# Optimization experiments

Measured on AMD Instinct MI355X. Metric: run time of the kernel, lower is better.

The kernel has to match this reference:

```python
import jax, jax.numpy as jnp
import numpy as np

B, T, D, H, L = 256, 1024, 64, 128, 2

def _lstm_layer(x, h0, c0, w_ih, w_hh, b):
    # x: [B,T,Din]; w_ih: [4H,Din]; w_hh: [4H,H]; b: [4H]
    xg = jnp.einsum('btd,gd->btg', x, w_ih) + b  # precompute input-to-gate GEMM: [B,T,4H]
    def step(carry, xt):
        h, c = carry
        g = xt + h @ w_hh.T                       # [B,4H], torch gate order i,f,g,o
        i, f, gg, o = jnp.split(g, 4, axis=-1)
        c = jax.nn.sigmoid(f) * c + jax.nn.sigmoid(i) * jnp.tanh(gg)
        h = jax.nn.sigmoid(o) * jnp.tanh(c)
        return (h, c), h
    _, hs = jax.lax.scan(step, (h0, c0), jnp.swapaxes(xg, 0, 1))  # hs: [T,B,H]
    return jnp.swapaxes(hs, 0, 1)


def setup_inputs() -> dict:
    key = jax.random.key(0)
    ks = jax.random.split(key, 12)
    s = 1.0 / np.sqrt(H)
    u = lambda k, shp: jax.random.uniform(k, shp, jnp.float32, -s, s)
    return {
        'x': jax.random.normal(ks[0], (B, T, D), jnp.float32),
        'h0': jax.random.normal(ks[1], (L, B, H), jnp.float32),
        'w_ih_0': u(ks[2], (4 * H, D)),
        'w_hh_0': u(ks[3], (4 * H, H)),
        'b_0': u(ks[4], (4 * H,)),
        'w_ih_1': u(ks[5], (4 * H, H)),
        'w_hh_1': u(ks[6], (4 * H, H)),
        'b_1': u(ks[7], (4 * H,)),
        'fc_w': u(ks[8], (1, H)),
        'fc_b': u(ks[9], (1,)),
    }


def reference(x, h0, w_ih_0, w_hh_0, b_0, w_ih_1, w_hh_1, b_1, fc_w, fc_b):
    c0 = jnp.zeros((x.shape[0], w_hh_0.shape[1]), x.dtype)  # c0 = zeros as in original
    h = _lstm_layer(x, h0[0], c0, w_ih_0, w_hh_0, b_0)
    h = _lstm_layer(h, h0[1], c0, w_ih_1, w_hh_1, b_1)
    return h[:, -1, :] @ fc_w.T + fc_b  # fc2 on last timestep -> [B,1]
```

## Files before the change

### kernel.cpp

```cpp
#include <hip/hip_runtime.h>
#include <math.h>

#define NB  256
#define T   1024
#define DIN 64
#define H   128
#define G4  512
#define NBT (NB * T)
#define TG4 (T * G4)

typedef __attribute__((ext_vector_type(4))) float    f32x4;
typedef __attribute__((ext_vector_type(8))) _Float16 f16x8;
typedef __attribute__((ext_vector_type(4))) _Float16 f16x4;
typedef __attribute__((ext_vector_type(2))) _Float16 f16x2;

#define DPPQ(v, CTRL) __int_as_float(__builtin_amdgcn_update_dpp(0, __float_as_int(v), (CTRL), 0xf, 0xf, true))
#define MFMA16(A, B, C) __builtin_amdgcn_mfma_f32_16x16x32_f16((A), (B), (C), 0, 0, 0)

__device__ __forceinline__ float tanhf_(float x) { return 2.0f / (1.0f + __expf(-2.0f * x)) - 1.0f; }

__device__ __forceinline__ void wg_barrier() {
    asm volatile("s_waitcnt lgkmcnt(0)" ::: "memory");
    __builtin_amdgcn_s_barrier();
}

__device__ __forceinline__ f16x8 cvt8(const float* p) {
    float4 v0 = *(const float4*)p;
    float4 v1 = *(const float4*)(p + 4);
    return (f16x8){(_Float16)v0.x, (_Float16)v0.y, (_Float16)v0.z, (_Float16)v0.w,
                   (_Float16)v1.x, (_Float16)v1.y, (_Float16)v1.z, (_Float16)v1.w};
}

template<int K, int AH>
__global__ __launch_bounds__(256, 2)
void gemm_pp(const void* __restrict__ A, const float* __restrict__ W,
             _Float16* __restrict__ O)
{
    __shared__ _Float16 __align__(16) sA[128][136];
    __shared__ _Float16 __align__(16) sW[128][72];

    const int m0 = blockIdx.x << 7;
    const int j = threadIdx.x;
    const int lane = j & 63, wv = j >> 6;
    const int wm = wv >> 1, wn = wv & 1;
    const int q = lane >> 4, n16 = lane & 15;
    const int bb = m0 >> 10, s0 = m0 & (T - 1);
    const size_t bO = (size_t)bb * TG4;

    if constexpr (AH) {
        const _Float16* Ah = (const _Float16*)A;
        #pragma unroll
        for (int it = 0; it < 8; ++it) {
            int idx = j + it * 256;
            int kp = idx & 63, sblk = idx >> 6;
            f16x8 xv8 = *(const f16x8*)(Ah + bO + (size_t)kp * 2048
                                        + (size_t)(s0 + sblk * 4) * 2);
            #pragma unroll
            for (int d = 0; d < 4; ++d)
                *(f16x2*)&sA[sblk * 4 + d][2 * kp] = (f16x2){xv8[2 * d], xv8[2 * d + 1]};
        }
    } else {
        const float* Af = (const float*)A;
        #pragma unroll
        for (int it = 0; it < 8; ++it) {
            int idx = j + it * 256;
            int r = idx >> 4, kc = (idx & 15) << 2;
            float4 va = *(const float4*)(Af + (size_t)(m0 + r) * K + kc);
            *(f16x4*)&sA[r][kc] = (f16x4){(_Float16)va.x, (_Float16)va.y,
                                          (_Float16)va.z, (_Float16)va.w};
        }
    }

    for (int nb = 0; nb < 4; ++nb) {
        f32x4 acc[4][4];
        #pragma unroll
        for (int a = 0; a < 4; ++a)
            #pragma unroll
            for (int bq = 0; bq < 4; ++bq) acc[a][bq] = (f32x4){0.f, 0.f, 0.f, 0.f};

        #pragma unroll
        for (int kp = 0; kp < K / 64; ++kp) {
            __syncthreads();
            #pragma unroll
            for (int it = 0; it < 8; ++it) {
                int idx = j + it * 256;
                int r = idx >> 4, kc = (idx & 15) << 2;
                int n = (nb << 7) + r, pn = (n & 3) * 128 + (n >> 2);
                float4 vw = *(const float4*)(W + (size_t)pn * K + kp * 64 + kc);
                *(f16x4*)&sW[r][kc] = (f16x4){(_Float16)vw.x, (_Float16)vw.y,
                                              (_Float16)vw.z, (_Float16)vw.w};
            }
            __syncthreads();
            #pragma unroll
            for (int kh = 0; kh < 2; ++kh) {
                const int kk = kh * 32 + q * 8;
                f16x8 a[4], bf[4];
                #pragma unroll
                for (int mt = 0; mt < 4; ++mt)
                    a[mt] = *(const f16x8*)&sA[wm * 64 + mt * 16 + n16][kp * 64 + kk];
                #pragma unroll
                for (int nt = 0; nt < 4; ++nt)
                    bf[nt] = *(const f16x8*)&sW[wn * 64 + nt * 16 + n16][kk];
                #pragma unroll
                for (int nt = 0; nt < 4; ++nt)
                    #pragma unroll
                    for (int mt = 0; mt < 4; ++mt)
                        acc[mt][nt] = MFMA16(a[mt], bf[nt], acc[mt][nt]);
            }
        }
        const int N0 = (nb << 7) + wn * 64;
        const int nA = N0 + n16, nBc = N0 + 32 + n16;
        const int grpA = (nA >> 7) * 64 + ((nA >> 5) & 3) * 16 + (nA & 15);
        const int grpB = (nBc >> 7) * 64 + ((nBc >> 5) & 3) * 16 + (nBc & 15);
        #pragma unroll
        for (int mt = 0; mt < 4; ++mt) {
            int srow = (m0 + wm * 64 + mt * 16 + q * 4) & (T - 1);
            f16x8 pkA = {(_Float16)acc[mt][0][0], (_Float16)acc[mt][1][0],
                         (_Float16)acc[mt][0][1], (_Float16)acc[mt][1][1],
                         (_Float16)acc[mt][0][2], (_Float16)acc[mt][1][2],
                         (_Float16)acc[mt][0][3], (_Float16)acc[mt][1][3]};
            f16x8 pkB = {(_Float16)acc[mt][2][0], (_Float16)acc[mt][3][0],
                         (_Float16)acc[mt][2][1], (_Float16)acc[mt][3][1],
                         (_Float16)acc[mt][2][2], (_Float16)acc[mt][3][2],
                         (_Float16)acc[mt][2][3], (_Float16)acc[mt][3][3]};
            *(f16x8*)(O + bO + (size_t)grpA * 2048 + (size_t)srow * 2) = pkA;
            *(f16x8*)(O + bO + (size_t)grpB * 2048 + (size_t)srow * 2) = pkB;
        }
    }
}

__global__ __launch_bounds__(256, 1)
void lstm_scan(const _Float16* __restrict__ xg, const float* __restrict__ whh,
               const float* __restrict__ bias, const float* __restrict__ h0g,
               _Float16* hist, const float* __restrict__ fcw,
               const float* __restrict__ fcb, float* __restrict__ out, int dofc)
{
    __shared__ _Float16 __align__(16) hb[2][128];
    __shared__ float lds_r[128];

    const int b = blockIdx.x;
    const int t = threadIdx.x;
    const int lane = t & 63, v = t >> 6;
    const int l15 = lane & 15, q = lane >> 4;
    const int u = l15 >> 2, gg = l15 & 3;

    f16x8 wf[8][4];
    #pragma unroll
    for (int jj = 0; jj < 8; ++jj) {
        const int n  = 128 * v + 16 * jj + l15;
        const int pn = (n & 3) * 128 + (n >> 2);
        const float* wr = whh + (size_t)pn * H;
        #pragma unroll
        for (int kt = 0; kt < 4; ++kt)
            wf[jj][kt] = cvt8(wr + 32 * kt + q * 8);
    }
    const int huA = 32 * v + 8 * q + u;
    const int huB = huA + 4;
    const float bjA = bias[gg * 128 + huA];
    const float bjB = bias[gg * 128 + huB];

    const bool  isg = (gg == 2);
    const float nsc = isg ? -2.0f : -1.0f;
    const float va  = isg ?  2.0f :  1.0f;
    const float vb  = isg ? -1.0f :  0.0f;
    const bool  sq0 = (q & 1) != 0;
    const bool  sq1 = (q & 2) != 0;
    const bool  wlane = gg < 2;
    const int   hu_own = wlane ? (gg ? huB : huA) : huA;

    if (t < H) hb[0][t] = (_Float16)h0g[(size_t)b * H + t];

    float cA = 0.f, cB = 0.f, hOwn = 0.f;

    const _Float16* xgp = xg + (size_t)b * TG4 + (size_t)(v * 64 + q * 16 + l15) * 2048;
    f16x8 xr0 = *(const f16x8*)(xgp + 0);
    f16x8 xr1 = *(const f16x8*)(xgp + 8);

    _Float16* hp = hist ? hist + (size_t)b * TG4 + (size_t)(hu_own >> 1) * 2048 + (hu_own & 1)
                        : (_Float16*)0;

    __syncthreads();

    const f32x4 z = (f32x4){0.f, 0.f, 0.f, 0.f};

    for (int sb = 0; sb < T; sb += 8) {
        #pragma unroll
        for (int ss = 0; ss < 8; ++ss) {
            const int s = sb + ss;
            const int p = s & 1;

            f16x8 xcur = (ss < 4) ? xr0 : xr1;
            float xA = (float)xcur[(ss & 3) * 2];
            float xB = (float)xcur[(ss & 3) * 2 + 1];

            f16x8 af[4];
            #pragma unroll
            for (int kt = 0; kt < 4; ++kt)
                af[kt] = *(const f16x8*)(&hb[p][32 * kt + q * 8]);

            f32x4 a[8];
            #pragma unroll
            for (int jj = 0; jj < 8; ++jj)
                a[jj] = MFMA16(af[0], wf[jj][0], z);
            #pragma unroll
            for (int kt = 1; kt < 4; ++kt)
                #pragma unroll
                for (int jj = 0; jj < 8; ++jj)
                    a[jj] = MFMA16(af[kt], wf[jj][kt], a[jj]);

            float gA = (sq0 ? (sq1 ? a[6][0] : a[2][0]) : (sq1 ? a[4][0] : a[0][0]))
                       + xA + bjA;
            float gB = (sq0 ? (sq1 ? a[7][0] : a[3][0]) : (sq1 ? a[5][0] : a[1][0]))
                       + xB + bjB;

            if (ss == 3) { int i0 = sb + 8;  if (i0 > T - 4) i0 = T - 4; xr0 = *(const f16x8*)(xgp + (size_t)i0 * 2); }
            if (ss == 7) { int i1 = sb + 12; if (i1 > T - 4) i1 = T - 4; xr1 = *(const f16x8*)(xgp + (size_t)i1 * 2); }

            float uA  = 1.0f / (1.0f + __expf(nsc * gA));
            float vlA = fmaf(uA, va, vb);
            float uB  = 1.0f / (1.0f + __expf(nsc * gB));
            float vlB = fmaf(uB, va, vb);

            float niA = DPPQ(vlA, 0x00), nfA = DPPQ(vlA, 0x55);
            float ngA = DPPQ(vlA, 0xAA), noA = DPPQ(vlA, 0xFF);
            float niB = DPPQ(vlB, 0x00), nfB = DPPQ(vlB, 0x55);
            float ngB = DPPQ(vlB, 0xAA), noB = DPPQ(vlB, 0xFF);

            cA = nfA * cA + niA * ngA;
            cB = nfB * cB + niB * ngB;

            if (wlane) {
                float cs = gg ? cB : cA;
                float ns = gg ? noB : noA;
                float h  = ns * tanhf_(cs);
                hOwn = h;
                hb[p ^ 1][hu_own] = (_Float16)h;
                if (hp) hp[(size_t)s * 2] = (_Float16)h;
            }

            wg_barrier();
        }
    }

    if (dofc) {
        if (wlane) lds_r[hu_own] = hOwn * fcw[hu_own];
        __syncthreads();
        if (t == 0) {
            float s_ = fcb[0];
            for (int k = 0; k < H; ++k) s_ += lds_r[k];
            out[b] = s_;
        }
    }
}

extern "C" void kernel_launch(void* const* d_in, const int* in_sizes, int n_in,
                              void* d_out, int out_size, void* d_ws, size_t ws_size,
                              hipStream_t stream)
{
    const float* x    = (const float*)d_in[0];
    const float* h0   = (const float*)d_in[1];
    const float* wih0 = (const float*)d_in[2];
    const float* whh0 = (const float*)d_in[3];
    const float* b0   = (const float*)d_in[4];
    const float* wih1 = (const float*)d_in[5];
    const float* whh1 = (const float*)d_in[6];
    const float* b1   = (const float*)d_in[7];
    const float* fcw  = (const float*)d_in[8];
    const float* fcb  = (const float*)d_in[9];
    float* out = (float*)d_out;

    _Float16* xg = (_Float16*)d_ws;

    gemm_pp<64, 0><<<NBT / 128, 256, 0, stream>>>(x, wih0, xg);
    lstm_scan<<<NB, 256, 0, stream>>>(xg, whh0, b0, h0, xg,
                                      nullptr, nullptr, nullptr, 0);
    gemm_pp<128, 1><<<NBT / 128, 256, 0, stream>>>(xg, wih1, xg);
    lstm_scan<<<NB, 256, 0, stream>>>(xg, whh1, b1, h0 + (size_t)NB * H,
                                      nullptr, fcw, fcb, out, 1);
}
```

Before: 1.280 ms.

## Split LSTM scan across 512 threads and fold bias into input GEMM

The recurrent scan kernel now runs 512 threads per batch row (8 waves), so each wave holds half as many W_hh fragments and issues 16 MFMAs per step instead of 32. Each lane now handles a single gate element instead of two. The gate bias is added in the input-projection GEMM epilogue instead of per step in the scan. This shortens the serial per-step critical path, at the cost of a wider workgroup barrier across 8 waves each step and bias being rounded into fp16 with the projection.

```diff
diff --git a/kernel.cpp b/kernel.cpp
--- a/kernel.cpp
+++ b/kernel.cpp
@@ -16,6 +16,7 @@
 
 #define DPPQ(v, CTRL) __int_as_float(__builtin_amdgcn_update_dpp(0, __float_as_int(v), (CTRL), 0xf, 0xf, true))
 #define MFMA16(A, B, C) __builtin_amdgcn_mfma_f32_16x16x32_f16((A), (B), (C), 0, 0, 0)
+#define PN(n) ((((n) & 3) * 128) + ((n) >> 2))
 
 __device__ __forceinline__ float tanhf_(float x) { return 2.0f / (1.0f + __expf(-2.0f * x)) - 1.0f; }
 
@@ -34,7 +35,7 @@
 template<int K, int AH>
 __global__ __launch_bounds__(256, 2)
 void gemm_pp(const void* __restrict__ A, const float* __restrict__ W,
-             _Float16* __restrict__ O)
+             const float* __restrict__ bias, _Float16* __restrict__ O)
 {
     __shared__ _Float16 __align__(16) sA[128][136];
     __shared__ _Float16 __align__(16) sW[128][72];
@@ -85,7 +86,7 @@
             for (int it = 0; it < 8; ++it) {
                 int idx = j + it * 256;
                 int r = idx >> 4, kc = (idx & 15) << 2;
-                int n = (nb << 7) + r, pn = (n & 3) * 128 + (n >> 2);
+                int n = (nb << 7) + r, pn = PN(n);
                 float4 vw = *(const float4*)(W + (size_t)pn * K + kp * 64 + kc);
                 *(f16x4*)&sW[r][kc] = (f16x4){(_Float16)vw.x, (_Float16)vw.y,
                                               (_Float16)vw.z, (_Float16)vw.w};
@@ -112,28 +113,32 @@
         const int nA = N0 + n16, nBc = N0 + 32 + n16;
         const int grpA = (nA >> 7) * 64 + ((nA >> 5) & 3) * 16 + (nA & 15);
         const int grpB = (nBc >> 7) * 64 + ((nBc >> 5) & 3) * 16 + (nBc & 15);
+        const float biA0 = bias[PN(N0 + n16)];
+        const float biA1 = bias[PN(N0 + 16 + n16)];
+        const float biB0 = bias[PN(N0 + 32 + n16)];
+        const float biB1 = bias[PN(N0 + 48 + n16)];
         #pragma unroll
         for (int mt = 0; mt < 4; ++mt) {
             int srow = (m0 + wm * 64 + mt * 16 + q * 4) & (T - 1);
-            f16x8 pkA = {(_Float16)acc[mt][0][0], (_Float16)acc[mt][1][0],
-                         (_Float16)acc[mt][0][1], (_Float16)acc[mt][1][1],
-                         (_Float16)acc[mt][0][2], (_Float16)acc[mt][1][2],
-                         (_Float16)acc[mt][0][3], (_Float16)acc[mt][1][3]};
-            f16x8 pkB = {(_Float16)acc[mt][2][0], (_Float16)acc[mt][3][0],
-                         (_Float16)acc[mt][2][1], (_Float16)acc[mt][3][1],
-                         (_Float16)acc[mt][2][2], (_Float16)acc[mt][3][2],
-                         (_Float16)acc[mt][2][3], (_Float16)acc[mt][3][3]};
+            f16x8 pkA = {(_Float16)(acc[mt][0][0] + biA0), (_Float16)(acc[mt][1][0] + biA1),
+                         (_Float16)(acc[mt][0][1] + biA0), (_Float16)(acc[mt][1][1] + biA1),
+                         (_Float16)(acc[mt][0][2] + biA0), (_Float16)(acc[mt][1][2] + biA1),
+                         (_Float16)(acc[mt][0][3] + biA0), (_Float16)(acc[mt][1][3] + biA1)};
+            f16x8 pkB = {(_Float16)(acc[mt][2][0] + biB0), (_Float16)(acc[mt][3][0] + biB1),
+                         (_Float16)(acc[mt][2][1] + biB0), (_Float16)(acc[mt][3][1] + biB1),
+                         (_Float16)(acc[mt][2][2] + biB0), (_Float16)(acc[mt][3][2] + biB1),
+                         (_Float16)(acc[mt][2][3] + biB0), (_Float16)(acc[mt][3][3] + biB1)};
             *(f16x8*)(O + bO + (size_t)grpA * 2048 + (size_t)srow * 2) = pkA;
             *(f16x8*)(O + bO + (size_t)grpB * 2048 + (size_t)srow * 2) = pkB;
         }
     }
 }
 
-__global__ __launch_bounds__(256, 1)
+__global__ __launch_bounds__(512, 1)
 void lstm_scan(const _Float16* __restrict__ xg, const float* __restrict__ whh,
-               const float* __restrict__ bias, const float* __restrict__ h0g,
-               _Float16* hist, const float* __restrict__ fcw,
-               const float* __restrict__ fcb, float* __restrict__ out, int dofc)
+               const float* __restrict__ h0g, _Float16* hist,
+               const float* __restrict__ fcw, const float* __restrict__ fcb,
+               float* __restrict__ out, int dofc)
 {
     __shared__ _Float16 __align__(16) hb[2][128];
     __shared__ float lds_r[128];
@@ -142,42 +147,40 @@
     const int t = threadIdx.x;
     const int lane = t & 63, v = t >> 6;
     const int l15 = lane & 15, q = lane >> 4;
-    const int u = l15 >> 2, gg = l15 & 3;
-
-    f16x8 wf[8][4];
+    const int gg = t & 3, hu = t >> 2;
+
+    f16x8 wf[4][4];
     #pragma unroll
-    for (int jj = 0; jj < 8; ++jj) {
-        const int n  = 128 * v + 16 * jj + l15;
-        const int pn = (n & 3) * 128 + (n >> 2);
+    for (int jj = 0; jj < 4; ++jj) {
+        const int n  = 64 * v + 16 * jj + l15;
+        const int pn = PN(n);
         const float* wr = whh + (size_t)pn * H;
         #pragma unroll
         for (int kt = 0; kt < 4; ++kt)
             wf[jj][kt] = cvt8(wr + 32 * kt + q * 8);
     }
-    const int huA = 32 * v + 8 * q + u;
-    const int huB = huA + 4;
-    const float bjA = bias[gg * 128 + huA];
-    const float bjB = bias[gg * 128 + huB];
 
     const bool  isg = (gg == 2);
     const float nsc = isg ? -2.0f : -1.0f;
     const float va  = isg ?  2.0f :  1.0f;
     const float vb  = isg ? -1.0f :  0.0f;
-    const bool  sq0 = (q & 1) != 0;
-    const bool  sq1 = (q & 2) != 0;
-    const bool  wlane = gg < 2;
-    const int   hu_own = wlane ? (gg ? huB : huA) : huA;
+    const bool  s4  = (lane & 16) != 0;
+    const bool  s5  = (lane & 32) != 0;
+    const bool  wlane = (gg == 0);
 
     if (t < H) hb[0][t] = (_Float16)h0g[(size_t)b * H + t];
 
-    float cA = 0.f, cB = 0.f, hOwn = 0.f;
-
-    const _Float16* xgp = xg + (size_t)b * TG4 + (size_t)(v * 64 + q * 16 + l15) * 2048;
+    float c = 0.f, hOwn = 0.f;
+
+    const int grp = (t >> 7) * 64 + ((t >> 5) & 3) * 16 + (t & 15);
+    const int e   = (t >> 4) & 1;
+    const _Float16* xgp = xg + (size_t)b * TG4 + (size_t)grp * 2048;
     f16x8 xr0 = *(const f16x8*)(xgp + 0);
     f16x8 xr1 = *(const f16x8*)(xgp + 8);
 
-    _Float16* hp = hist ? hist + (size_t)b * TG4 + (size_t)(hu_own >> 1) * 2048 + (hu_own & 1)
-                        : (_Float16*)0;
+    _Float16* hp = (hist && wlane)
+        ? hist + (size_t)b * TG4 + (size_t)(hu >> 1) * 2048 + (hu & 1)
+        : (_Float16*)0;
 
     __syncthreads();
 
@@ -190,51 +193,43 @@
             const int p = s & 1;
 
             f16x8 xcur = (ss < 4) ? xr0 : xr1;
-            float xA = (float)xcur[(ss & 3) * 2];
-            float xB = (float)xcur[(ss & 3) * 2 + 1];
+            const int k2 = (ss & 3) * 2;
+            float xv = e ? (float)xcur[k2 + 1] : (float)xcur[k2];
 
             f16x8 af[4];
             #pragma unroll
             for (int kt = 0; kt < 4; ++kt)
                 af[kt] = *(const f16x8*)(&hb[p][32 * kt + q * 8]);
 
-            f32x4 a[8];
-            #pragma unroll
-            for (int jj = 0; jj < 8; ++jj)
-                a[jj] = MFMA16(af[0], wf[jj][0], z);
-            #pragma unroll
-            for (int kt = 1; kt < 4; ++kt)
-                #pragma unroll
-                for (int jj = 0; jj < 8; ++jj)
-                    a[jj] = MFMA16(af[kt], wf[jj][kt], a[jj]);
-
-            float gA = (sq0 ? (sq1 ? a[6][0] : a[2][0]) : (sq1 ? a[4][0] : a[0][0]))
-                       + xA + bjA;
-            float gB = (sq0 ? (sq1 ? a[7][0] : a[3][0]) : (sq1 ? a[5][0] : a[1][0]))
-                       + xB + bjB;
+            f32x4 a0 = MFMA16(af[0], wf[0][0], z);
+            f32x4 a1 = MFMA16(af[0], wf[1][0], z);
+            f32x4 a2 = MFMA16(af[0], wf[2][0], z);
+            f32x4 a3 = MFMA16(af[0], wf[3][0], z);
+            #pragma unroll
+            for (int kt = 1; kt < 4; ++kt) {
+                a0 = MFMA16(af[kt], wf[0][kt], a0);
+                a1 = MFMA16(af[kt], wf[1][kt], a1);
+                a2 = MFMA16(af[kt], wf[2][kt], a2);
+                a3 = MFMA16(af[kt], wf[3][kt], a3);
+            }
 
             if (ss == 3) { int i0 = sb + 8;  if (i0 > T - 4) i0 = T - 4; xr0 = *(const f16x8*)(xgp + (size_t)i0 * 2); }
             if (ss == 7) { int i1 = sb + 12; if (i1 > T - 4) i1 = T - 4; xr1 = *(const f16x8*)(xgp + (size_t)i1 * 2); }
 
-            float uA  = 1.0f / (1.0f + __expf(nsc * gA));
-            float vlA = fmaf(uA, va, vb);
-            float uB  = 1.0f / (1.0f + __expf(nsc * gB));
-            float vlB = fmaf(uB, va, vb);
-
-            float niA = DPPQ(vlA, 0x00), nfA = DPPQ(vlA, 0x55);
-            float ngA = DPPQ(vlA, 0xAA), noA = DPPQ(vlA, 0xFF);
-            float niB = DPPQ(vlB, 0x00), nfB = DPPQ(vlB, 0x55);
-            float ngB = DPPQ(vlB, 0xAA), noB = DPPQ(vlB, 0xFF);
-
-            cA = nfA * cA + niA * ngA;
-            cB = nfB * cB + niB * ngB;
+            float own = s5 ? (s4 ? a3[0] : a2[0]) : (s4 ? a1[0] : a0[0]);
+            float g = own + xv;
+
+            float uu = 1.0f / (1.0f + __expf(nsc * g));
+            float vl = fmaf(uu, va, vb);
+
+            float ni = DPPQ(vl, 0x00), nf = DPPQ(vl, 0x55);
+            float ng = DPPQ(vl, 0xAA), no = DPPQ(vl, 0xFF);
+            c = nf * c + ni * ng;
 
             if (wlane) {
-                float cs = gg ? cB : cA;
-                float ns = gg ? noB : noA;
-                float h  = ns * tanhf_(cs);
+                float h = no * tanhf_(c);
                 hOwn = h;
-                hb[p ^ 1][hu_own] = (_Float16)h;
+                hb[p ^ 1][hu] = (_Float16)h;
                 if (hp) hp[(size_t)s * 2] = (_Float16)h;
             }
 
@@ -243,7 +238,7 @@
     }
 
     if (dofc) {
-        if (wlane) lds_r[hu_own] = hOwn * fcw[hu_own];
+        if (wlane) lds_r[hu] = hOwn * fcw[hu];
         __syncthreads();
         if (t == 0) {
             float s_ = fcb[0];
@@ -271,10 +266,10 @@
 
     _Float16* xg = (_Float16*)d_ws;
 
-    gemm_pp<64, 0><<<NBT / 128, 256, 0, stream>>>(x, wih0, xg);
-    lstm_scan<<<NB, 256, 0, stream>>>(xg, whh0, b0, h0, xg,
+    gemm_pp<64, 0><<<NBT / 128, 256, 0, stream>>>(x, wih0, b0, xg);
+    lstm_scan<<<NB, 512, 0, stream>>>(xg, whh0, h0, xg,
                                       nullptr, nullptr, nullptr, 0);
-    gemm_pp<128, 1><<<NBT / 128, 256, 0, stream>>>(xg, wih1, xg);
-    lstm_scan<<<NB, 256, 0, stream>>>(xg, whh1, b1, h0 + (size_t)NB * H,
+    gemm_pp<128, 1><<<NBT / 128, 256, 0, stream>>>(xg, wih1, b1, xg);
+    lstm_scan<<<NB, 512, 0, stream>>>(xg, whh1, h0 + (size_t)NB * H,
                                       nullptr, fcw, fcb, out, 1);
 }
```

After: 1.237 ms. 1.03x faster.
